# Kernel optimization log

Measured on AMD Instinct MI355X. Metric: run time of the kernel, lower is better.

## Reference

```python
import jax, jax.numpy as jnp
import numpy as np

HEADS, DIM_HEAD = 8, 64  # per init_kwargs


def cdist(x, w):
    """Euclidean distance between rows of x [..., n, d] and w [m, d] -> [..., n, m].
    Matches torch.cdist (non-squared) / L2DistanceLinear(squared=False)."""
    sq = (x * x).sum(-1, keepdims=True) + (w * w).sum(-1) - 2.0 * (x @ w.T)
    return jnp.sqrt(jnp.maximum(sq, 0.0))


def setup_inputs() -> dict:
    key = jax.random.key(0)
    k1, k2, k3 = jax.random.split(key, 3)
    B, N, D = 4, 2048, 512
    dim_inner = HEADS * DIM_HEAD  # 512
    x = jax.random.normal(k1, (B, N, D), dtype=jnp.float32)
    w_qkv = jax.random.normal(k2, (3 * dim_inner, D), dtype=jnp.float32)
    w_out = jax.random.normal(k3, (D, dim_inner), dtype=jnp.float32)
    return {"x": x, "w_qkv": w_qkv, "w_out": w_out}


def reference(x, w_qkv, w_out):
    B, N, D = x.shape
    scale = DIM_HEAD ** -0.5

    # L2-distance QKV projection (cdist, non-squared, no negate/bias)
    qkv = cdist(x, w_qkv)                                  # [B, N, 3*H*DH]
    qkv = qkv.reshape(B, N, 3, HEADS, DIM_HEAD).transpose(2, 0, 3, 1, 4)  # [3, B, H, N, DH]
    q, k, v = qkv[0], qkv[1], qkv[2]

    # neg squared-L2 attention scores: -(||q||^2 + ||k||^2 - 2 q.k)
    q_sq = (q * q).sum(-1)                                 # [B, H, N]
    k_sq = (k * k).sum(-1)                                 # [B, H, N]
    dots = jnp.einsum('bhid,bhjd->bhij', q, k)             # [B, H, N, N]
    sim = -(q_sq[..., :, None] + k_sq[..., None, :] - 2.0 * dots) * scale

    attn = jax.nn.softmax(sim, axis=-1)
    out = jnp.einsum('bhij,bhjd->bhid', attn, v)           # [B, H, N, DH]
    out = out.transpose(0, 2, 1, 3).reshape(B, N, HEADS * DIM_HEAD)

    # L2-distance output projection
    return cdist(out, w_out)                               # [B, N, D]
```

## Files before the change

### kernel.cpp

```cpp
#include <hip/hip_runtime.h>
#include <stdint.h>

typedef float v4f  __attribute__((ext_vector_type(4)));
typedef float v16f __attribute__((ext_vector_type(16)));
typedef short v8s  __attribute__((ext_vector_type(8)));
typedef uint32_t u32;

#define DEVI static __device__ __forceinline__

DEVI unsigned short f2bf(float f) {
    u32 u = __builtin_bit_cast(u32, f);
    u = (u + 0x7fffu + ((u >> 16) & 1u)) >> 16;
    return (unsigned short)u;
}
DEVI float bf2f(unsigned short h) {
    u32 u = ((u32)h) << 16;
    return __builtin_bit_cast(float, u);
}

template <typename T>
DEVI void async16(const T* g, T* l) {
    __builtin_amdgcn_global_load_lds(
        (const __attribute__((address_space(1))) u32*)g,
        (__attribute__((address_space(3))) u32*)l, 16, 0, 0);
}

DEVI v4f bmfma(v8s a, v8s b, v4f c) {
    return __builtin_amdgcn_mfma_f32_16x16x32_bf16(a, b, c, 0, 0, 0);
}
DEVI v16f bmfma32(v8s a, v8s b, v16f c) {
    return __builtin_amdgcn_mfma_f32_32x32x16_bf16(a, b, c, 0, 0, 0);
}

#if __has_builtin(__builtin_amdgcn_permlane32_swap)
#define HAVE_PLSWAP 1
typedef unsigned int v2u __attribute__((ext_vector_type(2)));
#endif

DEVI void swap32(u32 a, u32 b, u32& lo, u32& hi) {
#ifdef HAVE_PLSWAP
    v2u r = __builtin_amdgcn_permlane32_swap(a, b, false, false);
    lo = r.x; hi = r.y;
#else
    u32 ax = __shfl_xor(a, 32), bx = __shfl_xor(b, 32);
    int hh = (threadIdx.x & 63) >> 5;
    lo = hh ? bx : a;
    hi = hh ? b : ax;
#endif
}

static const size_t HSZ = 32ull * 2048 * 64;

__launch_bounds__(256, 2)
__global__ void prep_all(const float* __restrict__ X, const float* __restrict__ WQ,
                         const float* __restrict__ WO,
                         unsigned short* __restrict__ Xb, unsigned short* __restrict__ WQb,
                         unsigned short* __restrict__ WOb,
                         float* __restrict__ xsq, float* __restrict__ wqsq,
                         float* __restrict__ wosq, float* __restrict__ wors)
{
    const int bid = blockIdx.x;
    const int w = threadIdx.x >> 6, lane = threadIdx.x & 63;
    const float* src; unsigned short* dst; float* Sq; float* Rs = nullptr;
    int r;
    if (bid < 2048)      { src = X;  dst = Xb;  Sq = xsq;  r = bid * 4 + w; }
    else if (bid < 2432) { src = WQ; dst = WQb; Sq = wqsq; r = (bid - 2048) * 4 + w; }
    else                 { src = WO; dst = WOb; Sq = wosq; Rs = wors; r = (bid - 2432) * 4 + w; }

    const float* xr = src + (size_t)r * 512 + lane * 8;
    float4 a = *(const float4*)xr;
    float4 c = *(const float4*)(xr + 4);
    float s = a.x*a.x + a.y*a.y + a.z*a.z + a.w*a.w
            + c.x*c.x + c.y*c.y + c.z*c.z + c.w*c.w;
    float sm = a.x + a.y + a.z + a.w + c.x + c.y + c.z + c.w;
    uint4 pkv;
    unsigned short* e = (unsigned short*)&pkv;
    e[0] = f2bf(a.x); e[1] = f2bf(a.y); e[2] = f2bf(a.z); e[3] = f2bf(a.w);
    e[4] = f2bf(c.x); e[5] = f2bf(c.y); e[6] = f2bf(c.z); e[7] = f2bf(c.w);
    *(uint4*)(dst + (size_t)r * 512 + lane * 8) = pkv;
#pragma unroll
    for (int d = 32; d > 0; d >>= 1) {
        s  += __shfl_xor(s, d);
        sm += __shfl_xor(sm, d);
    }
    if (lane == 0) { Sq[r] = s; if (Rs) Rs[r] = sm; }
}

__launch_bounds__(256, 2)
__global__ void gemm_cdist(const unsigned short* __restrict__ A,
                           const unsigned short* __restrict__ B,
                           const float* __restrict__ Asq,
                           const float* __restrict__ Bsq,
                           unsigned short* __restrict__ QKV,
                           float* __restrict__ Ksqc)
{
    __shared__ unsigned short lsm[2 * 128 * 64];
    unsigned short* lA = lsm;
    unsigned short* lB = lsm + 128 * 64;
    const int t = threadIdx.x;
    const int lane = t & 63, w = t >> 6;
    const int low = lane & 15, quad = lane >> 4;
    const int wm = w & 1, wn = w >> 1;
    const int tM = blockIdx.x * 128, tN = blockIdx.y * 128;

    v4f acc[4][4];
#pragma unroll
    for (int a = 0; a < 4; ++a)
#pragma unroll
        for (int b = 0; b < 4; ++b) acc[a][b] = (v4f){0.f, 0.f, 0.f, 0.f};

    for (int kt = 0; kt < 512; kt += 64) {
        __syncthreads();
#pragma unroll
        for (int is = 0; is < 4; ++is) {
            int slot = is * 256 + t;
            int r = slot >> 3, bp = slot & 7;
            int bs = bp ^ (r & 7);
            async16(A + (size_t)(tM + r) * 512 + kt + bs * 8, lA + slot * 8);
            async16(B + (size_t)(tN + r) * 512 + kt + bs * 8, lB + slot * 8);
        }
        __syncthreads();

        v8s bfr[4][2];
#pragma unroll
        for (int ns = 0; ns < 4; ++ns) {
            int row = wn * 64 + ns * 16 + low;
#pragma unroll
            for (int kc = 0; kc < 2; ++kc)
                bfr[ns][kc] = *(const v8s*)(lB + (row * 8 + ((kc * 4 + quad) ^ (row & 7))) * 8);
        }
#pragma unroll
        for (int ms = 0; ms < 4; ++ms) {
            int row = wm * 64 + ms * 16 + low;
            v8s af0 = *(const v8s*)(lA + (row * 8 + ((0 + quad) ^ (row & 7))) * 8);
            v8s af1 = *(const v8s*)(lA + (row * 8 + ((4 + quad) ^ (row & 7))) * 8);
#pragma unroll
            for (int ns = 0; ns < 4; ++ns) {
                acc[ms][ns] = bmfma(af0, bfr[ns][0], acc[ms][ns]);
                acc[ms][ns] = bmfma(af1, bfr[ns][1], acc[ms][ns]);
            }
        }
    }

    const int tt = tN >> 9;
    if (tt != 2) {
#pragma unroll
        for (int ms = 0; ms < 4; ++ms) {
#pragma unroll
            for (int reg = 0; reg < 4; ++reg) {
                const int row = tM + wm * 64 + ms * 16 + quad * 4 + reg;
                const int b = row >> 11, i = row & 2047;
                float kacc = 0.f;
#pragma unroll
                for (int ns = 0; ns < 4; ++ns) {
                    const int col = tN + wn * 64 + ns * 16 + low;
                    float dot = acc[ms][ns][reg];
                    float val = sqrtf(fmaxf(Asq[row] + Bsq[col] - 2.f * dot, 0.f)) - 32.f;
                    int h = (col >> 6) & 7, d = col & 63, bh = b * 8 + h;
                    if (tt == 0) {
                        QKV[((size_t)bh * 2048 + i) * 64 + d] =
                            f2bf(val * 0.36067376022224085f);
                    } else {
                        QKV[HSZ + ((size_t)bh * 2048 + i) * 64 + d] = f2bf(val);
                        kacc += val * val;
                    }
                }
                if (tt == 1) {
#pragma unroll
                    for (int d = 1; d < 16; d <<= 1) kacc += __shfl_xor(kacc, d);
                    if (low == 0) {
                        int h = ((tN + wn * 64) >> 6) & 7;
                        Ksqc[(size_t)(b * 8 + h) * 2048 + i] = -kacc * 0.18033688011112042f;
                    }
                }
            }
        }
    } else {
        u32 packed[4][4][2];
#pragma unroll
        for (int ms = 0; ms < 4; ++ms)
#pragma unroll
            for (int ns = 0; ns < 4; ++ns) {
                const int col = tN + wn * 64 + ns * 16 + low;
                float bs_ = Bsq[col];
#pragma unroll
                for (int rp = 0; rp < 2; ++rp) {
                    u32 pk = 0;
#pragma unroll
                    for (int sub = 0; sub < 2; ++sub) {
                        int reg = rp * 2 + sub;
                        int row = tM + wm * 64 + ms * 16 + quad * 4 + reg;
                        float val = sqrtf(fmaxf(Asq[row] + bs_
                                                - 2.f * acc[ms][ns][reg], 0.f)) - 32.f;
                        pk |= (u32)f2bf(val) << (16 * sub);
                    }
                    packed[ms][ns][rp] = pk;
                }
            }
        u32* lT32 = (u32*)lsm;
#pragma unroll
        for (int p = 0; p < 2; ++p) {
            __syncthreads();
            if (wm == p) {
#pragma unroll
                for (int ms = 0; ms < 4; ++ms)
#pragma unroll
                    for (int ns = 0; ns < 4; ++ns) {
                        int cl = wn * 64 + ns * 16 + low;
#pragma unroll
                        for (int rp = 0; rp < 2; ++rp)
                            lT32[cl * 36 + ms * 8 + quad * 2 + rp] = packed[ms][ns][rp];
                    }
            }
            __syncthreads();
#pragma unroll
            for (int cc = 0; cc < 4; ++cc) {
                int col = cc * 32 + (t >> 3);
                int i0 = (t & 7) * 8;
                uint4 vvv = *(const uint4*)(lsm + col * 72 + i0);
                int colg = tN + col;
                int h = (colg >> 6) & 7, d = colg & 63;
                int rowg = tM + p * 64 + i0;
                int b = rowg >> 11, i = rowg & 2047;
                *(uint4*)(QKV + 2 * HSZ
                          + ((size_t)((b * 8 + h) * 64 + d)) * 2048 + i) = vvv;
            }
        }
    }
    (void)0;
}

__launch_bounds__(256, 2)
__global__ void flash_attn(const unsigned short* __restrict__ Q,
                           const unsigned short* __restrict__ K,
                           const unsigned short* __restrict__ VT,
                           const float* __restrict__ Ksqc,
                           unsigned short* __restrict__ PO,
                           float* __restrict__ PL)
{
    __shared__ unsigned short lK[2][64 * 64];
    __shared__ unsigned short lV[2][64 * 64];
    __shared__ float lKq[2][64];
    const int t = threadIdx.x, lane = t & 63, w = t >> 6;
    const int i31 = lane & 31, h = lane >> 5;
    const int qt = blockIdx.x, bh = blockIdx.y, sp = blockIdx.z;
    const size_t base = (size_t)bh * (2048 * 64);
    const int row0 = qt * 128 + w * 32;
    const int j0 = sp * 1024;

    v8s qfr[4];
#pragma unroll
    for (int kt = 0; kt < 4; ++kt)
        qfr[kt] = *(const v8s*)(Q + base + (size_t)(row0 + i31) * 64 + kt * 16 + h * 8);

    v16f o[2];
    float lacc = 0.f;
#pragma unroll
    for (int dt = 0; dt < 2; ++dt)
#pragma unroll
        for (int r = 0; r < 16; ++r) o[dt][r] = 0.f;

    const unsigned short* kg = K + base + (size_t)j0 * 64;
    const unsigned short* vg = VT + (size_t)bh * 64 * 2048 + j0;
    const float* kqg = Ksqc + (size_t)bh * 2048 + j0;

    auto STAGE = [&](int buf) {
#pragma unroll
        for (int is = 0; is < 2; ++is) {
            int slot = is * 256 + t;
            int r = slot >> 3, bp = slot & 7, bs = bp ^ (r & 7);
            async16(kg + (size_t)r * 64 + bs * 8, &lK[buf][slot * 8]);
        }
#pragma unroll
        for (int is = 0; is < 2; ++is) {
            int slot = is * 256 + t;
            int r = slot >> 3, bp = slot & 7, bs = bp ^ (r & 7);
            async16(vg + (size_t)r * 2048 + bs * 8, &lV[buf][slot * 8]);
        }
        if (t < 16) async16(kqg + t * 4, &lKq[buf][t * 4]);
        kg += 64 * 64; vg += 64; kqg += 64;
    };

    STAGE(0);
    __syncthreads();

#pragma unroll 2
    for (int iter = 0; iter < 16; ++iter) {
        const int c = iter & 1;
        if (iter < 15) STAGE(1 - c);

#pragma unroll
        for (int T = 0; T < 2; ++T) {
            const int jrow = T * 32 + i31;
            v8s kf[4];
#pragma unroll
            for (int kt = 0; kt < 4; ++kt)
                kf[kt] = *(const v8s*)(&lK[c][(jrow * 8 + ((2 * kt + h) ^ (jrow & 7))) * 8]);

            v16f sa;
#pragma unroll
            for (int r1 = 0; r1 < 4; ++r1) {
                v4f kq = *(const v4f*)(&lKq[c][T * 32 + r1 * 8 + h * 4]);
#pragma unroll
                for (int u = 0; u < 4; ++u) sa[4 * r1 + u] = kq[u];
            }
#pragma unroll
            for (int kt = 0; kt < 4; ++kt)
                sa = bmfma32(kf[kt], qfr[kt], sa);

            u32 pk[8];
#pragma unroll
            for (int r1 = 0; r1 < 4; ++r1) {
                float p0 = exp2f(sa[4 * r1 + 0]);
                float p1 = exp2f(sa[4 * r1 + 1]);
                float p2 = exp2f(sa[4 * r1 + 2]);
                float p3 = exp2f(sa[4 * r1 + 3]);
                lacc += (p0 + p1) + (p2 + p3);
                pk[2 * r1] = __builtin_amdgcn_perm(
                    __builtin_bit_cast(u32, p1), __builtin_bit_cast(u32, p0),
                    0x07060302u);
                pk[2 * r1 + 1] = __builtin_amdgcn_perm(
                    __builtin_bit_cast(u32, p3), __builtin_bit_cast(u32, p2),
                    0x07060302u);
            }
#pragma unroll
            for (int c2 = 0; c2 < 2; ++c2) {
                const int jb = 2 * (2 * T + c2);
                v8s vf[2];
#pragma unroll
                for (int dt = 0; dt < 2; ++dt) {
                    const int drow = dt * 32 + i31;
                    vf[dt] = *(const v8s*)(&lV[c][(drow * 8 + ((jb + h) ^ (drow & 7))) * 8]);
                }
                uint4 dd;
                swap32(pk[4 * c2 + 0], pk[4 * c2 + 2], dd.x, dd.z);
                swap32(pk[4 * c2 + 1], pk[4 * c2 + 3], dd.y, dd.w);
                v8s af = __builtin_bit_cast(v8s, dd);
                o[0] = bmfma32(af, vf[0], o[0]);
                o[1] = bmfma32(af, vf[1], o[1]);
            }
        }
        __syncthreads();
    }

    const int pb = (qt * 32 + bh) * 2 + sp;
    unsigned short* pob = PO + (size_t)pb * 8192;
    lacc += __shfl_xor(lacc, 32);
#pragma unroll
    for (int dt = 0; dt < 2; ++dt)
#pragma unroll
        for (int r = 0; r < 16; ++r) {
            int rl = w * 32 + (r & 3) + 8 * (r >> 2) + 4 * h;
            pob[rl * 64 + dt * 32 + i31] = f2bf(o[dt][r]);
        }
    if (h == 0)
        PL[(size_t)pb * 128 + w * 32 + i31] = lacc;
}

__launch_bounds__(256, 2)
__global__ void combine_kernel(const unsigned short* __restrict__ PO,
                               const float* __restrict__ PL,
                               unsigned short* __restrict__ O,
                               float* __restrict__ Osqp)
{
    const int qt = blockIdx.x, bh = blockIdx.y, t = threadIdx.x;
    const int b = bh >> 3, h = bh & 7;
    const int pbase = ((qt >> 1) * 32 + bh) * 2;
    const int rl = (qt & 1) * 64 + (t >> 2), c0 = (t & 3) * 16;
    float inv = 1.f / (PL[(size_t)pbase * 128 + rl] + PL[(size_t)(pbase + 1) * 128 + rl]);
    const unsigned short* a = PO + (size_t)pbase * 8192 + rl * 64 + c0;
    const unsigned short* bb = a + 8192;
    uint4 a0 = *(const uint4*)a,  a1 = *(const uint4*)(a + 8);
    uint4 b0 = *(const uint4*)bb, b1 = *(const uint4*)(bb + 8);
    const unsigned short* ae = (const unsigned short*)&a0;
    const unsigned short* be = (const unsigned short*)&b0;
    uint4 o0, o1;
    unsigned short* oe = (unsigned short*)&o0;
#pragma unroll
    for (int u = 0; u < 8; ++u) oe[u] = f2bf((bf2f(ae[u]) + bf2f(be[u])) * inv);
    ae = (const unsigned short*)&a1; be = (const unsigned short*)&b1;
    oe = (unsigned short*)&o1;
#pragma unroll
    for (int u = 0; u < 8; ++u) oe[u] = f2bf((bf2f(ae[u]) + bf2f(be[u])) * inv);
    unsigned short* dst = O + ((size_t)(b * 2048 + qt * 64 + (t >> 2))) * 512 + h * 64 + c0;
    *(uint4*)dst = o0;
    *(uint4*)(dst + 8) = o1;

    const unsigned short* q0 = (const unsigned short*)&o0;
    const unsigned short* q1 = (const unsigned short*)&o1;
    float s = 0.f;
#pragma unroll
    for (int u = 0; u < 8; ++u) { float f = bf2f(q0[u]) + 32.f; s += f * f; }
#pragma unroll
    for (int u = 0; u < 8; ++u) { float f = bf2f(q1[u]) + 32.f; s += f * f; }
    s += __shfl_xor(s, 1);
    s += __shfl_xor(s, 2);
    if ((t & 3) == 0)
        Osqp[(size_t)h * 8192 + b * 2048 + qt * 64 + (t >> 2)] = s;
}

__launch_bounds__(256, 2)
__global__ void gemm_out(const unsigned short* __restrict__ A,
                         const unsigned short* __restrict__ B,
                         const float* __restrict__ Osqp,
                         const float* __restrict__ Bsq,
                         const float* __restrict__ Brs,
                         float* __restrict__ OUT)
{
    __shared__ unsigned short lA[128 * 64];
    __shared__ unsigned short lB[64 * 64];
    __shared__ float lAsq[128];
    const int t = threadIdx.x;
    const int lane = t & 63, w = t >> 6;
    const int low = lane & 15, quad = lane >> 4;
    const int wm = w & 1, wn = w >> 1;
    const int tM = blockIdx.x * 128, tN = blockIdx.y * 64;

    if (t < 128) {
        float s = 0.f;
#pragma unroll
        for (int hh = 0; hh < 8; ++hh) s += Osqp[(size_t)hh * 8192 + tM + t];
        lAsq[t] = s;
    }

    v4f acc[4][2];
#pragma unroll
    for (int a = 0; a < 4; ++a)
#pragma unroll
        for (int b = 0; b < 2; ++b) acc[a][b] = (v4f){0.f, 0.f, 0.f, 0.f};

    for (int kt = 0; kt < 512; kt += 64) {
        __syncthreads();
#pragma unroll
        for (int is = 0; is < 4; ++is) {
            int slot = is * 256 + t;
            int r = slot >> 3, bp = slot & 7, bs = bp ^ (r & 7);
            async16(A + (size_t)(tM + r) * 512 + kt + bs * 8, lA + slot * 8);
        }
#pragma unroll
        for (int is = 0; is < 2; ++is) {
            int slot = is * 256 + t;
            int r = slot >> 3, bp = slot & 7, bs = bp ^ (r & 7);
            async16(B + (size_t)(tN + r) * 512 + kt + bs * 8, lB + slot * 8);
        }
        __syncthreads();

        v8s bfr[2][2];
#pragma unroll
        for (int ns = 0; ns < 2; ++ns) {
            int row = wn * 32 + ns * 16 + low;
#pragma unroll
            for (int kc = 0; kc < 2; ++kc)
                bfr[ns][kc] = *(const v8s*)(lB + (row * 8 + ((kc * 4 + quad) ^ (row & 7))) * 8);
        }
#pragma unroll
        for (int ms = 0; ms < 4; ++ms) {
            int row = wm * 64 + ms * 16 + low;
            v8s af0 = *(const v8s*)(lA + (row * 8 + ((0 + quad) ^ (row & 7))) * 8);
            v8s af1 = *(const v8s*)(lA + (row * 8 + ((4 + quad) ^ (row & 7))) * 8);
#pragma unroll
            for (int ns = 0; ns < 2; ++ns) {
                acc[ms][ns] = bmfma(af0, bfr[ns][0], acc[ms][ns]);
                acc[ms][ns] = bmfma(af1, bfr[ns][1], acc[ms][ns]);
            }
        }
    }

#pragma unroll
    for (int ms = 0; ms < 4; ++ms) {
#pragma unroll
        for (int ns = 0; ns < 2; ++ns) {
#pragma unroll
            for (int reg = 0; reg < 4; ++reg) {
                int rloc = wm * 64 + ms * 16 + quad * 4 + reg;
                int row = tM + rloc;
                int col = tN + wn * 32 + ns * 16 + low;
                float val = sqrtf(fmaxf(lAsq[rloc] + Bsq[col]
                                        - 2.f * (acc[ms][ns][reg] + 32.f * Brs[col]), 0.f));
                OUT[(size_t)row * 512 + col] = val;
            }
        }
    }
}

extern "C" void kernel_launch(void* const* d_in, const int* in_sizes, int n_in,
                              void* d_out, int out_size, void* d_ws, size_t ws_size,
                              hipStream_t stream)
{
    const float* x    = (const float*)d_in[0];
    const float* wqkv = (const float*)d_in[1];
    const float* wout = (const float*)d_in[2];
    float* out = (float*)d_out;

    char* ws = (char*)d_ws;
    size_t off = 0;
    auto alloc = [&](size_t bytes) -> void* {
        void* p = ws + off;
        off += (bytes + 255) & ~(size_t)255;
        return p;
    };
    unsigned short* xb   = (unsigned short*)alloc(8192ull * 512 * 2);
    unsigned short* wqb  = (unsigned short*)alloc(1536ull * 512 * 2);
    unsigned short* wob  = (unsigned short*)alloc(512ull * 512 * 2);
    unsigned short* qkv  = (unsigned short*)alloc(3ull * HSZ * 2);
    unsigned short* outp = (unsigned short*)alloc(8192ull * 512 * 2);
    unsigned short* po   = (unsigned short*)alloc(1024ull * 8192 * 2);
    float* pl   = (float*)alloc(1024ull * 128 * 4);
    float* xsq  = (float*)alloc(8192 * 4);
    float* wqsq = (float*)alloc(1536 * 4);
    float* wosq = (float*)alloc(512 * 4);
    float* wors = (float*)alloc(512 * 4);
    float* ksqc = (float*)alloc(65536ull * 4);
    float* osqp = (float*)alloc(8ull * 8192 * 4);

    prep_all<<<2560, 256, 0, stream>>>(x, wqkv, wout, xb, wqb, wob,
                                       xsq, wqsq, wosq, wors);

    gemm_cdist<<<dim3(64, 12), 256, 0, stream>>>(xb, wqb, xsq, wqsq, qkv, ksqc);
    flash_attn<<<dim3(16, 32, 2), 256, 0, stream>>>(qkv, qkv + HSZ, qkv + 2 * HSZ,
                                                    ksqc, po, pl);
    combine_kernel<<<dim3(32, 32), 256, 0, stream>>>(po, pl, outp, osqp);
    gemm_out<<<dim3(64, 8), 256, 0, stream>>>(outp, wob, osqp, wosq, wors, out);
}
```

Before: 173.1 us.

## Double-buffer LDS tiles in both GEMMs and raise MFMA priority in attention

The QKV cdist GEMM now splits K into 32-wide stages held in two LDS buffers, with a 4-way XOR swizzle, so the async global-to-LDS load of the next stage overlaps the MFMAs on the current one. The output GEMM gets the same two-buffer ping-pong at 64-wide stages. Each iteration drops one of its two barriers. The attention kernel wraps its MFMA/exp section in s_setprio(1)/s_setprio(0) to favour compute waves. LDS use per block stays the same in the QKV GEMM and doubles in the output GEMM, which could lower occupancy there. The shorter K stages in the QKV GEMM also double the number of loop iterations and barriers.

```diff
diff --git a/kernel.cpp b/kernel.cpp
--- a/kernel.cpp
+++ b/kernel.cpp
@@ -94,9 +94,7 @@
                            unsigned short* __restrict__ QKV,
                            float* __restrict__ Ksqc)
 {
-    __shared__ unsigned short lsm[2 * 128 * 64];
-    unsigned short* lA = lsm;
-    unsigned short* lB = lsm + 128 * 64;
+    __shared__ unsigned short lsm[2 * 2 * 128 * 32];
     const int t = threadIdx.x;
     const int lane = t & 63, w = t >> 6;
     const int low = lane & 15, quad = lane >> 4;
@@ -109,37 +107,45 @@
 #pragma unroll
         for (int b = 0; b < 4; ++b) acc[a][b] = (v4f){0.f, 0.f, 0.f, 0.f};
 
-    for (int kt = 0; kt < 512; kt += 64) {
-        __syncthreads();
-#pragma unroll
-        for (int is = 0; is < 4; ++is) {
+    int kstage = 0;
+    auto STAGE = [&](int buf) {
+        unsigned short* lA = lsm + buf * 8192;
+        unsigned short* lB = lA + 4096;
+#pragma unroll
+        for (int is = 0; is < 2; ++is) {
             int slot = is * 256 + t;
-            int r = slot >> 3, bp = slot & 7;
-            int bs = bp ^ (r & 7);
-            async16(A + (size_t)(tM + r) * 512 + kt + bs * 8, lA + slot * 8);
-            async16(B + (size_t)(tN + r) * 512 + kt + bs * 8, lB + slot * 8);
-        }
-        __syncthreads();
-
-        v8s bfr[4][2];
+            int r = slot >> 2, bp = slot & 3, bs = bp ^ (r & 3);
+            async16(A + (size_t)(tM + r) * 512 + kstage + bs * 8, lA + slot * 8);
+            async16(B + (size_t)(tN + r) * 512 + kstage + bs * 8, lB + slot * 8);
+        }
+        kstage += 32;
+    };
+
+    STAGE(0);
+    __syncthreads();
+
+#pragma unroll 2
+    for (int iter = 0; iter < 16; ++iter) {
+        const int c = iter & 1;
+        if (iter < 15) STAGE(1 - c);
+        const unsigned short* lA = lsm + c * 8192;
+        const unsigned short* lB = lA + 4096;
+
+        v8s bfr[4];
 #pragma unroll
         for (int ns = 0; ns < 4; ++ns) {
             int row = wn * 64 + ns * 16 + low;
-#pragma unroll
-            for (int kc = 0; kc < 2; ++kc)
-                bfr[ns][kc] = *(const v8s*)(lB + (row * 8 + ((kc * 4 + quad) ^ (row & 7))) * 8);
+            bfr[ns] = *(const v8s*)(lB + (row * 4 + (quad ^ (row & 3))) * 8);
         }
 #pragma unroll
         for (int ms = 0; ms < 4; ++ms) {
             int row = wm * 64 + ms * 16 + low;
-            v8s af0 = *(const v8s*)(lA + (row * 8 + ((0 + quad) ^ (row & 7))) * 8);
-            v8s af1 = *(const v8s*)(lA + (row * 8 + ((4 + quad) ^ (row & 7))) * 8);
-#pragma unroll
-            for (int ns = 0; ns < 4; ++ns) {
-                acc[ms][ns] = bmfma(af0, bfr[ns][0], acc[ms][ns]);
-                acc[ms][ns] = bmfma(af1, bfr[ns][1], acc[ms][ns]);
-            }
-        }
+            v8s af = *(const v8s*)(lA + (row * 4 + (quad ^ (row & 3))) * 8);
+#pragma unroll
+            for (int ns = 0; ns < 4; ++ns)
+                acc[ms][ns] = bmfma(af, bfr[ns], acc[ms][ns]);
+        }
+        __syncthreads();
     }
 
     const int tt = tN >> 9;
@@ -304,10 +310,10 @@
 #pragma unroll
                 for (int u = 0; u < 4; ++u) sa[4 * r1 + u] = kq[u];
             }
+            __builtin_amdgcn_s_setprio(1);
 #pragma unroll
             for (int kt = 0; kt < 4; ++kt)
                 sa = bmfma32(kf[kt], qfr[kt], sa);
-
             u32 pk[8];
 #pragma unroll
             for (int r1 = 0; r1 < 4; ++r1) {
@@ -339,6 +345,7 @@
                 o[0] = bmfma32(af, vf[0], o[0]);
                 o[1] = bmfma32(af, vf[1], o[1]);
             }
+            __builtin_amdgcn_s_setprio(0);
         }
         __syncthreads();
     }
@@ -407,8 +414,8 @@
                          const float* __restrict__ Brs,
                          float* __restrict__ OUT)
 {
-    __shared__ unsigned short lA[128 * 64];
-    __shared__ unsigned short lB[64 * 64];
+    __shared__ unsigned short lA[2][128 * 64];
+    __shared__ unsigned short lB[2][64 * 64];
     __shared__ float lAsq[128];
     const int t = threadIdx.x;
     const int lane = t & 63, w = t >> 6;
@@ -429,21 +436,30 @@
 #pragma unroll
         for (int b = 0; b < 2; ++b) acc[a][b] = (v4f){0.f, 0.f, 0.f, 0.f};
 
-    for (int kt = 0; kt < 512; kt += 64) {
-        __syncthreads();
+    int kstage = 0;
+    auto STAGE = [&](int buf) {
 #pragma unroll
         for (int is = 0; is < 4; ++is) {
             int slot = is * 256 + t;
             int r = slot >> 3, bp = slot & 7, bs = bp ^ (r & 7);
-            async16(A + (size_t)(tM + r) * 512 + kt + bs * 8, lA + slot * 8);
+            async16(A + (size_t)(tM + r) * 512 + kstage + bs * 8, &lA[buf][slot * 8]);
         }
 #pragma unroll
         for (int is = 0; is < 2; ++is) {
             int slot = is * 256 + t;
             int r = slot >> 3, bp = slot & 7, bs = bp ^ (r & 7);
-            async16(B + (size_t)(tN + r) * 512 + kt + bs * 8, lB + slot * 8);
-        }
-        __syncthreads();
+            async16(B + (size_t)(tN + r) * 512 + kstage + bs * 8, &lB[buf][slot * 8]);
+        }
+        kstage += 64;
+    };
+
+    STAGE(0);
+    __syncthreads();
+
+#pragma unroll 2
+    for (int iter = 0; iter < 8; ++iter) {
+        const int c = iter & 1;
+        if (iter < 7) STAGE(1 - c);
 
         v8s bfr[2][2];
 #pragma unroll
@@ -451,19 +467,20 @@
             int row = wn * 32 + ns * 16 + low;
 #pragma unroll
             for (int kc = 0; kc < 2; ++kc)
-                bfr[ns][kc] = *(const v8s*)(lB + (row * 8 + ((kc * 4 + quad) ^ (row & 7))) * 8);
+                bfr[ns][kc] = *(const v8s*)(&lB[c][(row * 8 + ((kc * 4 + quad) ^ (row & 7))) * 8]);
         }
 #pragma unroll
         for (int ms = 0; ms < 4; ++ms) {
             int row = wm * 64 + ms * 16 + low;
-            v8s af0 = *(const v8s*)(lA + (row * 8 + ((0 + quad) ^ (row & 7))) * 8);
-            v8s af1 = *(const v8s*)(lA + (row * 8 + ((4 + quad) ^ (row & 7))) * 8);
+            v8s af0 = *(const v8s*)(&lA[c][(row * 8 + ((0 + quad) ^ (row & 7))) * 8]);
+            v8s af1 = *(const v8s*)(&lA[c][(row * 8 + ((4 + quad) ^ (row & 7))) * 8]);
 #pragma unroll
             for (int ns = 0; ns < 2; ++ns) {
                 acc[ms][ns] = bmfma(af0, bfr[ns][0], acc[ms][ns]);
                 acc[ms][ns] = bmfma(af1, bfr[ns][1], acc[ms][ns]);
             }
         }
+        __syncthreads();
     }
 
 #pragma unroll
```

After: 174.8 us. No clear change (+1.0%).
